# Optimization experiments

Measured on AMD Instinct MI355X. Metric: run time of the kernel, lower is better.

Reference implementation:

```python
import jax, jax.numpy as jnp
import numpy as np

B, T, D, H, K = 128, 64, 2048, 512, 512
WINDOWS = [2, 3, 4]
ROUT = 2 * H            # bidirectional GRU output dim = 1024
FIN = ROUT + len(WINDOWS) * K + 2048 + 1024  # 5632 ('full' concat)
FOUT = 2048
BN_EPS = 1e-5


def setup_inputs() -> dict:
    key = jax.random.key(0)
    ks = jax.random.split(key, 32)
    s = 0.02
    inp = {
        "videos": jax.random.normal(ks[0], (B, T, D), jnp.float32),
        "motions": jax.random.normal(ks[1], (B, 1024), jnp.float32),
        "videos_origin": jax.random.normal(ks[2], (B, 2048), jnp.float32),
        "lengths": jax.random.randint(ks[3], (B,), 1, T + 1, jnp.int32),
        # GRU params (PyTorch layout: gates ordered r,z,n stacked on dim 0)
        "Wih_f": jax.random.normal(ks[4], (3 * H, D), jnp.float32) * s,
        "Whh_f": jax.random.normal(ks[5], (3 * H, H), jnp.float32) * s,
        "bih_f": jnp.zeros((3 * H,), jnp.float32),
        "bhh_f": jnp.zeros((3 * H,), jnp.float32),
        "Wih_b": jax.random.normal(ks[6], (3 * H, D), jnp.float32) * s,
        "Whh_b": jax.random.normal(ks[7], (3 * H, H), jnp.float32) * s,
        "bih_b": jnp.zeros((3 * H,), jnp.float32),
        "bhh_b": jnp.zeros((3 * H,), jnp.float32),
        # FC + BatchNorm1d (eval-mode) of MFC
        "fc_w": jax.random.normal(ks[8], (FOUT, FIN), jnp.float32) * (np.sqrt(6.0) / np.sqrt(FIN + FOUT)),
        "fc_b": jnp.zeros((FOUT,), jnp.float32),
        "bn_gamma": jnp.ones((FOUT,), jnp.float32),
        "bn_beta": jnp.zeros((FOUT,), jnp.float32),
        "bn_mean": jnp.zeros((FOUT,), jnp.float32),
        "bn_var": jnp.ones((FOUT,), jnp.float32),
    }
    for i, ws in enumerate(WINDOWS):
        inp[f"conv_w{ws}"] = jax.random.normal(ks[10 + 2 * i], (K, 1, ws, ROUT), jnp.float32) * s
        inp[f"conv_b{ws}"] = jnp.zeros((K,), jnp.float32)
    # mask consistent with lengths: mask[b,t] = t < lengths[b]
    inp["videos_mask"] = (jnp.arange(T)[None, :] < inp["lengths"][:, None]).astype(jnp.float32)
    return inp


def _gru_dir(x, Wih, Whh, bih, bhh, reverse):
    # x: [B,T,D] -> outputs [B,T,H]; torch GRU cell with r,z,n gate order
    xg = jnp.einsum("btd,gd->btg", x, Wih) + bih  # [B,T,3H] precomputed input gates

    def step(h, xg_t):
        hg = h @ Whh.T + bhh
        xr, xz, xn = jnp.split(xg_t, 3, axis=-1)
        hr, hz, hn = jnp.split(hg, 3, axis=-1)
        r = jax.nn.sigmoid(xr + hr)
        z = jax.nn.sigmoid(xz + hz)
        n = jnp.tanh(xn + r * hn)
        h_new = (1.0 - z) * n + z * h
        return h_new, h_new

    h0 = jnp.zeros((x.shape[0], Whh.shape[1]), x.dtype)
    _, hs = jax.lax.scan(step, h0, jnp.swapaxes(xg, 0, 1), reverse=reverse)
    return jnp.swapaxes(hs, 0, 1)


def _conv_branch(x4, w, b, ws):
    # x4: [B,1,T,ROUT], w: [K,1,ws,ROUT]; torch padding=(ws-1, 0)
    y = jax.lax.conv_general_dilated(
        x4, w, (1, 1), [(ws - 1, ws - 1), (0, 0)],
        dimension_numbers=("NCHW", "OIHW", "NCHW"))  # [B,K,T+ws-1,1]
    y = jax.nn.relu(y + b[None, :, None, None])
    return jnp.max(y, axis=(2, 3))  # max_pool1d over full time -> [B,K]


def _forward(videos, motions, videos_origin, lengths, videos_mask,
             Wih_f, Whh_f, bih_f, bhh_f, Wih_b, Whh_b, bih_b, bhh_b,
             conv_w2, conv_b2, conv_w3, conv_b3, conv_w4, conv_b4,
             fc_w, fc_b, bn_gamma, bn_beta, bn_mean, bn_var):
    fwd = _gru_dir(videos, Wih_f, Whh_f, bih_f, bhh_f, reverse=False)
    bwd = _gru_dir(videos, Wih_b, Whh_b, bih_b, bhh_b, reverse=True)
    gru_init_out = jnp.concatenate([fwd, bwd], axis=-1)  # [B,T,2H]

    # masked mean over valid frames (vectorized version of the batch for-loop)
    denom = lengths.astype(gru_init_out.dtype)[:, None]
    gru_out = jnp.sum(gru_init_out * videos_mask[:, :, None], axis=1) / denom  # [B,2H]

    masked = gru_init_out * videos_mask[:, :, None]
    x4 = masked[:, None, :, :]  # [B,1,T,2H]
    con_out = jnp.concatenate([
        _conv_branch(x4, conv_w2, conv_b2, 2),
        _conv_branch(x4, conv_w3, conv_b3, 3),
        _conv_branch(x4, conv_w4, conv_b4, 4),
    ], axis=1)  # [B,3K]

    # concate == 'full' (dropout is identity in eval)
    features = jnp.concatenate([gru_out, con_out, videos_origin, motions], axis=1)
    features = features @ fc_w.T + fc_b
    # BatchNorm1d, eval mode with running stats
    features = bn_gamma * (features - bn_mean) * jax.lax.rsqrt(bn_var + BN_EPS) + bn_beta
    # l2norm over dim 1
    features = features / jnp.sqrt(jnp.sum(features * features, axis=1, keepdims=True))
    return features


def reference(videos, motions, videos_origin, lengths, videos_mask,
              Wih_f, Whh_f, bih_f, bhh_f, Wih_b, Whh_b, bih_b, bhh_b,
              conv_w2, conv_b2, conv_w3, conv_b3, conv_w4, conv_b4,
              fc_w, fc_b, bn_gamma, bn_beta, bn_mean, bn_var):
    return _forward(videos, motions, videos_origin, lengths, videos_mask,
                    Wih_f, Whh_f, bih_f, bhh_f, Wih_b, Whh_b, bih_b, bhh_b,
                    conv_w2, conv_b2, conv_w3, conv_b3, conv_w4, conv_b4,
                    fc_w, fc_b, bn_gamma, bn_beta, bn_mean, bn_var)
```

## Files before the change

kernel.cpp:

```cpp
#include <hip/hip_runtime.h>
#include <hip/hip_bf16.h>
#include <stdint.h>

typedef __attribute__((ext_vector_type(8))) short short8;
typedef __attribute__((ext_vector_type(4))) float floatx4;
typedef __attribute__((ext_vector_type(4))) unsigned int u32x4;
typedef unsigned short u16;
typedef unsigned int u32;
typedef unsigned long long u64;

static __device__ __forceinline__ u16 f2bf(float f) {
  union { float f; u32 u; } v; v.f = f;
  return (u16)((v.u + 0x7fffu + ((v.u >> 16) & 1u)) >> 16);
}
static __device__ __forceinline__ float bf2f(u16 h) {
  union { u32 u; float f; } v; v.u = ((u32)h) << 16; return v.f;
}
static __device__ __forceinline__ u64 pack4(float a, float b, float c, float d) {
  return (u64)f2bf(a) | ((u64)f2bf(b) << 16) | ((u64)f2bf(c) << 32) | ((u64)f2bf(d) << 48);
}

__global__ __launch_bounds__(256) void k_pre_cvt(
    const float* __restrict__ videos, const float* __restrict__ Wih_f,
    const float* __restrict__ Wih_b, const float* __restrict__ Whh_f,
    const float* __restrict__ Whh_b, const float* __restrict__ bih_f,
    const float* __restrict__ bih_b, const float* __restrict__ fcb,
    const float* __restrict__ gam, const float* __restrict__ bet,
    const float* __restrict__ mu, const float* __restrict__ var,
    u16* __restrict__ vid, u16* __restrict__ wih, u16* __restrict__ whh,
    float* __restrict__ bihcat, float* __restrict__ bns, float* __restrict__ bnt)
{
  const int O1 = 4194304;
  const int O2 = O1 + 786432;
  const int O3 = O2 + 786432;
  const int O4 = O3 + 196608;
  const int O5 = O4 + 196608;
  const int NQ = O5 + 1280;
  for (int q = blockIdx.x * 256 + threadIdx.x; q < NQ; q += gridDim.x * 256) {
    if (q < O1) {
      float4 v = ((const float4*)videos)[q];
      ((u64*)vid)[q] = pack4(v.x, v.y, v.z, v.w);
    } else if (q < O2) {
      int r = q - O1; float4 v = ((const float4*)Wih_f)[r];
      ((u64*)wih)[r] = pack4(v.x, v.y, v.z, v.w);
    } else if (q < O3) {
      int r = q - O2; float4 v = ((const float4*)Wih_b)[r];
      ((u64*)wih)[r + 786432] = pack4(v.x, v.y, v.z, v.w);
    } else if (q < O4) {
      int r = q - O3; float4 v = ((const float4*)Whh_f)[r];
      ((u64*)whh)[r] = pack4(v.x, v.y, v.z, v.w);
    } else if (q < O5) {
      int r = q - O4; float4 v = ((const float4*)Whh_b)[r];
      ((u64*)whh)[r + 196608] = pack4(v.x, v.y, v.z, v.w);
    } else {
      int r = q - O5;
      if (r < 768) {
        int i = r * 4;
        const float* s = (i < 1536) ? (bih_f + i) : (bih_b + (i - 1536));
        *(float4*)&bihcat[i] = *(const float4*)s;
      } else {
        int i = (r - 768) * 4;
#pragma unroll
        for (int j = 0; j < 4; ++j) {
          int idx = i + j;
          float sc = gam[idx] * rsqrtf(var[idx] + 1e-5f);
          bns[idx] = sc;
          bnt[idx] = sc * (fcb[idx] - mu[idx]) + bet[idx];
        }
      }
    }
  }
}

static __device__ __forceinline__ void gload_lds16(const u16* g, u16* l) {
  __builtin_amdgcn_global_load_lds((const __attribute__((address_space(1))) u32*)(const void*)g,
                                   (__attribute__((address_space(3))) u32*)(void*)l, 16, 0, 0);
}

static __device__ __forceinline__ void stage_half_256(
    const u16* __restrict__ Mat, long K, int rowbase, int ktile, u16* lregion,
    int tid, int wid)
{
  int srow = tid >> 3;
  int sce = (((tid >> 3) ^ tid) & 7) * 8;
  const u16* g0 = Mat + (long)(rowbase + srow) * K + ktile * 64 + sce;
  const u16* g1 = Mat + (long)(rowbase + 64 + srow) * K + ktile * 64 + sce;
  gload_lds16(g0, lregion + wid * 512);
  gload_lds16(g1, lregion + 4096 + wid * 512);
}

__global__ __launch_bounds__(512) void gemm256(
    const u16* __restrict__ A, const u16* __restrict__ Bm,
    float* __restrict__ C, u16* __restrict__ C16, int M, int N, int K, int NT,
    const float* __restrict__ shift)
{
  __shared__ u16 lds[65536];
  int tid = threadIdx.x, lane = tid & 63, wid = tid >> 6;
  int r16 = lane & 15, kq = lane >> 4;
  int wr = wid >> 2, wc = wid & 3;
  int nwg = gridDim.x * gridDim.y;
  int lin = blockIdx.y * gridDim.x + blockIdx.x;
  int q8 = nwg >> 3;
  int swz = (lin & 7) * q8 + (lin >> 3);
  int m0 = (swz / gridDim.x) * 256, n0 = (swz % gridDim.x) * 256;

  int fxor = (r16 & 7) << 4;
  int c0 = (kq * 16) ^ fxor;
  int c1 = c0 ^ 64;
  int brow0 = (wc & 1) * 64;
  const char* ldsc = (const char*)lds;

  const floatx4 z4 = {0.f, 0.f, 0.f, 0.f};
  floatx4 acc[8][4];
#pragma unroll
  for (int i = 0; i < 8; ++i)
#pragma unroll
    for (int j = 0; j < 4; ++j) acc[i][j] = z4;

  stage_half_256(Bm, K, n0,       0, lds,                 tid, wid);
  stage_half_256(Bm, K, n0 + 128, 0, lds + 8192,          tid, wid);
  stage_half_256(A,  K, m0,       0, lds + 16384,         tid, wid);
  stage_half_256(A,  K, m0 + 128, 0, lds + 24576,         tid, wid);
  stage_half_256(Bm, K, n0,       1, lds + 32768,         tid, wid);
  stage_half_256(Bm, K, n0 + 128, 1, lds + 32768 + 8192,  tid, wid);
  stage_half_256(A,  K, m0,       1, lds + 32768 + 16384, tid, wid);
  stage_half_256(A,  K, m0 + 128, 1, lds + 32768 + 24576, tid, wid);
  asm volatile("s_waitcnt vmcnt(8)" ::: "memory");
  asm volatile("s_barrier" ::: "memory");

#define MFMA_CLUSTER(q)                                                        \
  asm volatile("s_waitcnt lgkmcnt(0)" ::: "memory");                           \
  __builtin_amdgcn_sched_barrier(0);                                           \
  __builtin_amdgcn_s_setprio(1);                                               \
  _Pragma("unroll")                                                            \
  for (int s = 0; s < 2; ++s)                                                  \
    _Pragma("unroll")                                                          \
    for (int e = 0; e < 2; ++e)                                                \
      _Pragma("unroll")                                                        \
      for (int j = 0; j < 4; ++j)                                              \
        acc[(q)*2 + e][j] = __builtin_amdgcn_mfma_f32_16x16x32_bf16(           \
            af[e][s], bf[j][s], acc[(q)*2 + e][j], 0, 0, 0);                   \
  __builtin_amdgcn_s_setprio(0);

  for (int T = 0; T < NT; ++T) {
    int P = T & 1;
    int Tn1 = (T + 1 < NT) ? T + 1 : 0;
    int Tn2 = (T + 2 < NT) ? T + 2 : T + 2 - NT;
    const char* bbase = ldsc + P * 65536 + (wc >> 1) * 16384;
    const char* abase = ldsc + P * 65536 + 32768 + wr * 16384;
    short8 bf[4][2];
    {
#pragma unroll
      for (int j = 0; j < 4; ++j) {
        bf[j][0] = *(const short8*)(bbase + (brow0 + j * 16 + r16) * 128 + c0);
        bf[j][1] = *(const short8*)(bbase + (brow0 + j * 16 + r16) * 128 + c1);
      }
      short8 af[2][2];
#pragma unroll
      for (int e = 0; e < 2; ++e) {
        af[e][0] = *(const short8*)(abase + (e * 16 + r16) * 128 + c0);
        af[e][1] = *(const short8*)(abase + (e * 16 + r16) * 128 + c1);
      }
      stage_half_256(A, K, m0, Tn1, lds + (Tn1 & 1) * 32768 + 16384, tid, wid);
      asm volatile("s_barrier" ::: "memory");
      MFMA_CLUSTER(0)
      asm volatile("s_barrier" ::: "memory");
    }
    {
      short8 af[2][2];
#pragma unroll
      for (int e = 0; e < 2; ++e) {
        af[e][0] = *(const short8*)(abase + ((2 + e) * 16 + r16) * 128 + c0);
        af[e][1] = *(const short8*)(abase + ((2 + e) * 16 + r16) * 128 + c1);
      }
      stage_half_256(A, K, m0 + 128, Tn1, lds + (Tn1 & 1) * 32768 + 24576, tid, wid);
      asm volatile("s_barrier" ::: "memory");
      MFMA_CLUSTER(1)
      asm volatile("s_barrier" ::: "memory");
    }
    {
      short8 af[2][2];
#pragma unroll
      for (int e = 0; e < 2; ++e) {
        af[e][0] = *(const short8*)(abase + ((4 + e) * 16 + r16) * 128 + c0);
        af[e][1] = *(const short8*)(abase + ((4 + e) * 16 + r16) * 128 + c1);
      }
      stage_half_256(Bm, K, n0, Tn2, lds + P * 32768, tid, wid);
      asm volatile("s_barrier" ::: "memory");
      MFMA_CLUSTER(2)
      asm volatile("s_barrier" ::: "memory");
    }
    {
      short8 af[2][2];
#pragma unroll
      for (int e = 0; e < 2; ++e) {
        af[e][0] = *(const short8*)(abase + ((6 + e) * 16 + r16) * 128 + c0);
        af[e][1] = *(const short8*)(abase + ((6 + e) * 16 + r16) * 128 + c1);
      }
      stage_half_256(Bm, K, n0 + 128, Tn2, lds + P * 32768 + 8192, tid, wid);
      asm volatile("s_barrier" ::: "memory");
      MFMA_CLUSTER(3)
      asm volatile("s_waitcnt vmcnt(4)" ::: "memory");
      asm volatile("s_barrier" ::: "memory");
    }
  }
#undef MFMA_CLUSTER

#pragma unroll
  for (int mf = 0; mf < 8; ++mf)
#pragma unroll
    for (int j = 0; j < 4; ++j) {
      int col = n0 + wc * 64 + j * 16 + r16;
      int row = m0 + wr * 128 + mf * 16 + kq * 4;
      if (C16) {
#pragma unroll
        for (int qq = 0; qq < 4; ++qq)
          C16[(long)(row + qq) * N + col] = f2bf(acc[mf][j][qq]);
      } else {
        float sh = shift ? shift[col] : 0.f;
#pragma unroll
        for (int qq = 0; qq < 4; ++qq)
          C[(long)(row + qq) * N + col] = acc[mf][j][qq] + sh;
      }
    }
}

__global__ __launch_bounds__(256) void gemm_bt(
    const u16* __restrict__ A, const u16* __restrict__ Bm,
    float* __restrict__ C, u16* __restrict__ C16, int M, int N, int K, int kn,
    const float* __restrict__ scale, const float* __restrict__ shift)
{
  __shared__ u16 As[128 * 32];
  __shared__ u16 Bs[128 * 32];
  int tid = threadIdx.x, lane = tid & 63, wid = tid >> 6;
  int nwg = gridDim.x * gridDim.y;
  int lin = blockIdx.y * gridDim.x + blockIdx.x;
  int q8 = nwg >> 3;
  int swz = (lin & 7) * q8 + (lin >> 3);
  int m0 = (swz / gridDim.x) * 128, n0 = (swz % gridDim.x) * 128;
  int kt0 = blockIdx.z * kn;
  int wr = wid >> 1, wc = wid & 1;
  int r16 = lane & 15, kq = lane >> 4;
  const floatx4 z4 = {0.f, 0.f, 0.f, 0.f};
  floatx4 acc[4][4];
#pragma unroll
  for (int i = 0; i < 4; ++i)
#pragma unroll
    for (int j = 0; j < 4; ++j) acc[i][j] = z4;
  for (int kt = kt0; kt < kt0 + kn; ++kt) {
    __syncthreads();
#pragma unroll
    for (int inst = 0; inst < 2; ++inst) {
      int g = inst * 256 + tid;
      int row = g >> 2, cb = g & 3;
      const u16* ga = A + (long)(m0 + row) * K + kt * 32 + cb * 8;
      const u16* gb = Bm + (long)(n0 + row) * K + kt * 32 + cb * 8;
      gload_lds16(ga, &As[(inst * 256 + wid * 64) * 8]);
      gload_lds16(gb, &Bs[(inst * 256 + wid * 64) * 8]);
    }
    __syncthreads();
    short8 af[4], bf[4];
#pragma unroll
    for (int mt = 0; mt < 4; ++mt) af[mt] = *(const short8*)&As[(wr * 64 + mt * 16 + r16) * 32 + kq * 8];
#pragma unroll
    for (int nt = 0; nt < 4; ++nt) bf[nt] = *(const short8*)&Bs[(wc * 64 + nt * 16 + r16) * 32 + kq * 8];
#pragma unroll
    for (int mt = 0; mt < 4; ++mt)
#pragma unroll
      for (int nt = 0; nt < 4; ++nt)
        acc[mt][nt] = __builtin_amdgcn_mfma_f32_16x16x32_bf16(af[mt], bf[nt], acc[mt][nt], 0, 0, 0);
  }
  float* Cp = C + (long)blockIdx.z * M * N;
#pragma unroll
  for (int nt = 0; nt < 4; ++nt) {
    int col = n0 + wc * 64 + nt * 16 + r16;
    float sc = scale ? scale[col] : 1.f;
    float sh = shift ? shift[col] : 0.f;
#pragma unroll
    for (int mt = 0; mt < 4; ++mt)
#pragma unroll
      for (int q = 0; q < 4; ++q) {
        int row = m0 + wr * 64 + mt * 16 + kq * 4 + q;
        float v = acc[mt][nt][q] * sc + sh;
        if (C16) C16[(long)row * N + col] = f2bf(v);
        else     Cp[(long)row * N + col] = v;
      }
  }
}

__global__ __launch_bounds__(512) void gru_rec(
    const float* __restrict__ xg,
    const u16* __restrict__ whhb,
    const float* __restrict__ bhh_f, const float* __restrict__ bhh_b,
    u16* __restrict__ hbuf,
    u16* __restrict__ maskb,
    u16* __restrict__ feat,
    const int* __restrict__ lengths,
    int* __restrict__ flg,
    const float* __restrict__ fc_w, const float* __restrict__ w2,
    const float* __restrict__ w3, const float* __restrict__ w4,
    const float* __restrict__ vo, const float* __restrict__ mo,
    u16* __restrict__ fcw, u16* __restrict__ wc)
{
  __shared__ float part[2][4][3][256];
  __shared__ u16 hstage[8192];
  int tid = threadIdx.x, lane = tid & 63, wid = tid >> 6;
  int bid = blockIdx.x;

  if (bid >= 128) {
    int cid = bid - 128;
    const int C1 = 2883584;
    const int C2 = C1 + 1179648;
    const int C3 = C2 + 65536;
    const int NQ = C3 + 32768;
    for (int q = cid * 512 + tid; q < NQ; q += 128 * 512) {
      if (q < C1) {
        float4 v = ((const float4*)fc_w)[q];
        ((u64*)fcw)[q] = pack4(v.x, v.y, v.z, v.w);
      } else if (q < C2) {
        int r = q - C1;
        int e = r << 2;
        int row = e >> 10, col = e & 1023;
        const float* src;
        if (row < 1024)      { int j = row >> 9, k = row & 511;                 src = w2 + (k * 2 + j) * 1024; }
        else if (row < 2560) { int m = row - 1024; int j = m >> 9, k = m & 511; src = w3 + (k * 3 + j) * 1024; }
        else                 { int m = row - 2560; int j = m >> 9, k = m & 511; src = w4 + (k * 4 + j) * 1024; }
        float4 v = *(const float4*)(src + col);
        ((u64*)wc)[r] = pack4(v.x, v.y, v.z, v.w);
      } else if (q < C3) {
        int r = q - C2; int b = r >> 9, c = (r & 511) * 4;
        float4 v = *(const float4*)&vo[(long)b * 2048 + c];
        *(u64*)&feat[(long)b * 5632 + 2560 + c] = pack4(v.x, v.y, v.z, v.w);
      } else {
        int r = q - C3; int b = r >> 8, c = (r & 255) * 4;
        float4 v = *(const float4*)&mo[(long)b * 1024 + c];
        *(u64*)&feat[(long)b * 5632 + 4608 + c] = pack4(v.x, v.y, v.z, v.w);
      }
    }
    return;
  }

  int dir = bid >> 6, rem = bid & 63, bt = rem >> 3, is = rem & 7;
  int ih = wid & 3, ks = wid >> 2;
  int gbase = (dir * 8 + bt) * 32;
  int r16 = lane & 15, kq = lane >> 4;
  int iglob = is * 64 + ih * 16 + r16;
  int i0 = is * 64 + ih * 16 + kq * 4;
  int batch = bt * 16 + r16;
  int pollidx = gbase + (lane & 31);
  int pubidx = gbase + is * 4 + ih;
  const float* bhh = dir ? bhh_b : bhh_f;
  const floatx4 z4 = {0.f, 0.f, 0.f, 0.f};
  int len = lengths[batch];

  short8 wfrag[3][8];
#pragma unroll
  for (int g = 0; g < 3; ++g) {
    const u16* wrow = whhb + (long)(dir * 1536 + g * 512 + iglob) * 512;
#pragma unroll
    for (int kk = 0; kk < 8; ++kk)
      wfrag[g][kk] = *(const short8*)&wrow[(ks * 8 + kk) * 32 + kq * 8];
  }
  float4 bh4[3];
#pragma unroll
  for (int g = 0; g < 3; ++g) bh4[g] = *(const float4*)&bhh[g * 512 + i0];
  float4 hprev = {0.f, 0.f, 0.f, 0.f};
  float4 msum = {0.f, 0.f, 0.f, 0.f};

  float4 px[3];
  if (ks == 0) {
    int ts0 = dir ? 63 : 0;
    long xb = (long)(batch * 64 + ts0) * 3072 + dir * 1536 + i0;
#pragma unroll
    for (int g = 0; g < 3; ++g) px[g] = *(const float4*)&xg[xb + g * 512];
  }

  int so0 = wid * 2048 + lane * 16;
  int so1 = so0 + 1024;
  char* sl0 = (char*)hstage + (so0 ^ (((so0 >> 10) & 7) << 4));
  char* sl1 = (char*)hstage + (so1 ^ (((so1 >> 10) & 7) << 4));
  int rb = r16 * 1024 + ks * 512 + kq * 16;
  int rsw = (r16 & 7) << 4;

  for (int t = 0; t < 64; ++t) {
    if (t > 0) {
      if (wid == 0) {
        while (true) {
          int v;
          asm volatile("global_load_dword %0, %1, off sc0 sc1\n\ts_waitcnt vmcnt(0)"
                       : "=v"(v) : "v"(&flg[pollidx]) : "memory");
          if (__all(v >= t)) break;
          __builtin_amdgcn_s_sleep(1);
        }
      }
      asm volatile("s_barrier" ::: "memory");
    }
    int par = t & 1;
    const char* hsrc = (const char*)(hbuf + (long)((par * 2 + dir) * 128 + bt * 16) * 512);
    u32x4 qa, qb;
    asm volatile(
      "global_load_dwordx4 %0, %2, off sc0 sc1\n\t"
      "global_load_dwordx4 %1, %3, off sc0 sc1"
      : "=&v"(qa), "=&v"(qb)
      : "v"(hsrc + so0), "v"(hsrc + so1)
      : "memory");
    asm volatile("s_waitcnt vmcnt(0)" ::: "memory");
    *(u32x4*)sl0 = qa;
    *(u32x4*)sl1 = qb;
    float4 pxn[3];
    if (ks == 0 && t < 63) {
      int ts1 = dir ? (62 - t) : (t + 1);
      long xb = (long)(batch * 64 + ts1) * 3072 + dir * 1536 + i0;
#pragma unroll
      for (int g = 0; g < 3; ++g) pxn[g] = *(const float4*)&xg[xb + g * 512];
    }
    asm volatile("s_waitcnt lgkmcnt(0)\n\ts_barrier" ::: "memory");
    floatx4 acc[3];
#pragma unroll
    for (int g = 0; g < 3; ++g) acc[g] = z4;
#pragma unroll
    for (int kk = 0; kk < 8; ++kk) {
      short8 hv = *(const short8*)((const char*)hstage + ((rb + kk * 64) ^ rsw));
#pragma unroll
      for (int g = 0; g < 3; ++g)
        acc[g] = __builtin_amdgcn_mfma_f32_16x16x32_bf16(wfrag[g][kk], hv, acc[g], 0, 0, 0);
    }
    if (ks == 1) {
#pragma unroll
      for (int g = 0; g < 3; ++g) *(floatx4*)&part[par][ih][g][lane * 4] = acc[g];
    }
    asm volatile("s_waitcnt lgkmcnt(0)\n\ts_barrier" ::: "memory");
    if (ks == 0) {
      int tsrc = dir ? (63 - t) : t;
#pragma unroll
      for (int g = 0; g < 3; ++g) acc[g] += *(const floatx4*)&part[par][ih][g][lane * 4];
      float4 hn4;
#pragma unroll
      for (int q = 0; q < 4; ++q) {
        float rr = acc[0][q] + ((const float*)&bh4[0])[q] + ((const float*)&px[0])[q];
        float zz = acc[1][q] + ((const float*)&bh4[1])[q] + ((const float*)&px[1])[q];
        float r = 1.f / (1.f + __expf(-rr));
        float z = 1.f / (1.f + __expf(-zz));
        float n = tanhf(((const float*)&px[2])[q] + r * (acc[2][q] + ((const float*)&bh4[2])[q]));
        ((float*)&hn4)[q] = (1.f - z) * n + z * ((const float*)&hprev)[q];
      }
      hprev = hn4;
      u16* hdst = hbuf + (long)(((par ^ 1) * 2 + dir) * 128 + bt * 16) * 512;
      u64 hval = pack4(hn4.x, hn4.y, hn4.z, hn4.w);
      asm volatile("global_atomic_swap_x2 %0, %1, off sc1"
                   :: "v"((u64*)&hdst[r16 * 512 + i0]), "v"(hval) : "memory");
      if (t < 63) {
        asm volatile("s_waitcnt vmcnt(0)" ::: "memory");
        if (lane == 0) {
          int tv = t + 1;
          asm volatile("global_atomic_swap %0, %1, off sc1"
                       :: "v"(&flg[pubidx]), "v"(tv) : "memory");
        }
      }
      bool mv = tsrc < len;
      *(u64*)&maskb[(long)(batch * 64 + tsrc) * 1024 + dir * 512 + i0] = mv ? hval : 0ull;
      if (mv) {
        msum.x += hn4.x; msum.y += hn4.y; msum.z += hn4.z; msum.w += hn4.w;
      }
      px[0] = pxn[0]; px[1] = pxn[1]; px[2] = pxn[2];
    }
  }
  if (ks == 0) {
    float inv = 1.0f / (float)len;
    *(u64*)&feat[(long)batch * 5632 + dir * 512 + i0] =
        pack4(msum.x * inv, msum.y * inv, msum.z * inv, msum.w * inv);
  }
}

__global__ __launch_bounds__(256) void k_conv_finish(
    const u16* __restrict__ z, const float* __restrict__ cb2,
    const float* __restrict__ cb3, const float* __restrict__ cb4,
    u16* __restrict__ feat)
{
  int b = blockIdx.x, wsi = blockIdx.y, k2 = threadIdx.x * 2;
  int ws = wsi + 2;
  int base = (wsi == 0) ? 0 : (wsi == 1 ? 1024 : 2560);
  const float* cb = (wsi == 0) ? cb2 : (wsi == 1 ? cb3 : cb4);
  float bias0 = cb[k2], bias1 = cb[k2 + 1];
  float m0 = 0.f, m1 = 0.f;
  for (int p = 0; p < 64 + ws - 1; ++p) {
    float a0 = bias0, a1 = bias1;
    for (int j = 0; j < ws; ++j) {
      int t = p - (ws - 1) + j;
      if (t >= 0 && t < 64) {
        u32 v = *(const u32*)&z[(long)(b * 64 + t) * 4608 + base + j * 512 + k2];
        a0 += bf2f((u16)v);
        a1 += bf2f((u16)(v >> 16));
      }
    }
    m0 = fmaxf(m0, a0);
    m1 = fmaxf(m1, a1);
  }
  *(u32*)&feat[(long)b * 5632 + 1024 + wsi * 512 + k2] = (u32)f2bf(m0) | ((u32)f2bf(m1) << 16);
}

__global__ __launch_bounds__(256) void k_l2norm(const float* __restrict__ p,
    const float* __restrict__ bns, const float* __restrict__ bnt, float* __restrict__ out)
{
  __shared__ float red[4];
  int b = blockIdx.x, tid = threadIdx.x;
  float v[8]; float s = 0.f;
#pragma unroll
  for (int j = 0; j < 8; ++j) {
    int i = j * 256 + tid;
    long o = (long)b * 2048 + i;
    float a = 0.f;
#pragma unroll
    for (int zz = 0; zz < 8; ++zz) a += p[o + (long)zz * 262144];
    a = a * bns[i] + bnt[i];
    v[j] = a; s += a * a;
  }
#pragma unroll
  for (int o = 32; o > 0; o >>= 1) s += __shfl_down(s, o);
  if ((tid & 63) == 0) red[tid >> 6] = s;
  __syncthreads();
  float rn = rsqrtf(red[0] + red[1] + red[2] + red[3]);
#pragma unroll
  for (int j = 0; j < 8; ++j)
    out[(long)b * 2048 + j * 256 + tid] = v[j] * rn;
}

extern "C" void kernel_launch(void* const* d_in, const int* in_sizes, int n_in,
                              void* d_out, int out_size, void* d_ws, size_t ws_size,
                              hipStream_t stream)
{
  (void)in_sizes; (void)n_in; (void)out_size; (void)ws_size;
  const float* videos       = (const float*)d_in[0];
  const float* motions      = (const float*)d_in[1];
  const float* videos_origin= (const float*)d_in[2];
  const int*   lengths      = (const int*)d_in[3];
  const float* Wih_f = (const float*)d_in[4];
  const float* Whh_f = (const float*)d_in[5];
  const float* bih_f = (const float*)d_in[6];
  const float* bhh_f = (const float*)d_in[7];
  const float* Wih_b = (const float*)d_in[8];
  const float* Whh_b = (const float*)d_in[9];
  const float* bih_b = (const float*)d_in[10];
  const float* bhh_b = (const float*)d_in[11];
  const float* fc_w  = (const float*)d_in[12];
  const float* fc_b  = (const float*)d_in[13];
  const float* bn_gamma = (const float*)d_in[14];
  const float* bn_beta  = (const float*)d_in[15];
  const float* bn_mean  = (const float*)d_in[16];
  const float* bn_var   = (const float*)d_in[17];
  const float* conv_w2 = (const float*)d_in[18];
  const float* conv_b2 = (const float*)d_in[19];
  const float* conv_w3 = (const float*)d_in[20];
  const float* conv_b3 = (const float*)d_in[21];
  const float* conv_w4 = (const float*)d_in[22];
  const float* conv_b4 = (const float*)d_in[23];
  float* out = (float*)d_out;
  char* w = (char*)d_ws;

  const size_t XG    = 0;
  const size_t VID   = 134217728;
  const size_t MASKB = 167772160;
  const size_t WIH   = 184549376;
  const size_t WHH   = 197132288;
  const size_t WC    = 200278016;
  const size_t FCW   = 209715200;
  const size_t FEAT  = 232783872;
  const size_t BIH   = 235274240;
  const size_t BNS   = 235286528;
  const size_t BNT   = 235294720;
  const size_t HB    = 235302912;
  const size_t FLG   = HB + 524288;

  float* xg   = (float*)(w + XG);
  u16*   zb16 = (u16*)(w + XG);
  u16* vid    = (u16*)(w + VID);
  u16* maskb  = (u16*)(w + MASKB);
  float* fcp  = (float*)(w + MASKB);
  u16* wih    = (u16*)(w + WIH);
  u16* whh    = (u16*)(w + WHH);
  u16* wc_    = (u16*)(w + WC);
  u16* fcw    = (u16*)(w + FCW);
  u16* feat   = (u16*)(w + FEAT);
  float* bih  = (float*)(w + BIH);
  float* bns  = (float*)(w + BNS);
  float* bnt  = (float*)(w + BNT);
  u16* hb     = (u16*)(w + HB);
  int* flg    = (int*)(w + FLG);

  hipMemsetAsync(w + HB, 0, 524288 + 2048, stream);

  k_pre_cvt<<<4096, 256, 0, stream>>>(
      videos, Wih_f, Wih_b, Whh_f, Whh_b, bih_f, bih_b,
      fc_b, bn_gamma, bn_beta, bn_mean, bn_var,
      vid, wih, whh, bih, bns, bnt);

  gemm256<<<dim3(12, 32), 512, 0, stream>>>(vid, wih, xg, nullptr, 8192, 3072, 2048, 32, bih);

  {
    const float* xg_c = xg; const u16* whh_c = whh;
    u16* hb_c = hb; u16* mb_c = maskb; u16* ft_c = feat;
    const int* len_c = lengths; int* flg_c = flg;
    const float* bf_c = bhh_f; const float* bb_c = bhh_b;
    const float* fw_c = fc_w; const float* w2_c = conv_w2;
    const float* w3_c = conv_w3; const float* w4_c = conv_w4;
    const float* vo_c = videos_origin; const float* mo_c = motions;
    u16* fcw_c = fcw; u16* wc_c = wc_;
    void* args[] = { (void*)&xg_c, (void*)&whh_c, (void*)&bf_c, (void*)&bb_c,
                     (void*)&hb_c, (void*)&mb_c, (void*)&ft_c, (void*)&len_c, (void*)&flg_c,
                     (void*)&fw_c, (void*)&w2_c, (void*)&w3_c, (void*)&w4_c,
                     (void*)&vo_c, (void*)&mo_c, (void*)&fcw_c, (void*)&wc_c };
    hipLaunchCooperativeKernel(reinterpret_cast<void*>(gru_rec), dim3(256), dim3(512), args, 0, stream);
  }

  gemm256<<<dim3(18, 32), 512, 0, stream>>>(maskb, wc_, nullptr, zb16, 8192, 4608, 1024, 16, nullptr);
  k_conv_finish<<<dim3(128, 3), 256, 0, stream>>>(zb16, conv_b2, conv_b3, conv_b4, feat);
  gemm_bt<<<dim3(16, 1, 8), 256, 0, stream>>>(feat, fcw, fcp, nullptr, 128, 2048, 5632, 22, nullptr, nullptr);
  k_l2norm<<<128, 256, 0, stream>>>(fcp, bns, bnt, out);
}
```

Baseline: 592.7 us.

## Tag hidden-state words with step counter to replace separate flag polling

The GRU recurrence previously published each step's hidden state and then, after a vmcnt wait, a separate per-group flag that consumers polled before loading the state. Now every 32-bit pair of bf16 hidden values is stored alongside its step tag in one 64-bit atomic swap. Consumers spin directly on the data loads until all tags match the current step. This removes the wait-then-flag round trip and the separate poll from the critical path of each serial step, at the cost of doubling the hidden-state buffer size and having all threads spin on data.

```diff
diff --git a/kernel.cpp b/kernel.cpp
--- a/kernel.cpp
+++ b/kernel.cpp
@@ -292,11 +292,10 @@
     const float* __restrict__ xg,
     const u16* __restrict__ whhb,
     const float* __restrict__ bhh_f, const float* __restrict__ bhh_b,
-    u16* __restrict__ hbuf,
+    char* __restrict__ hb3,
     u16* __restrict__ maskb,
     u16* __restrict__ feat,
     const int* __restrict__ lengths,
-    int* __restrict__ flg,
     const float* __restrict__ fc_w, const float* __restrict__ w2,
     const float* __restrict__ w3, const float* __restrict__ w4,
     const float* __restrict__ vo, const float* __restrict__ mo,
@@ -342,13 +341,10 @@
 
   int dir = bid >> 6, rem = bid & 63, bt = rem >> 3, is = rem & 7;
   int ih = wid & 3, ks = wid >> 2;
-  int gbase = (dir * 8 + bt) * 32;
   int r16 = lane & 15, kq = lane >> 4;
   int iglob = is * 64 + ih * 16 + r16;
   int i0 = is * 64 + ih * 16 + kq * 4;
   int batch = bt * 16 + r16;
-  int pollidx = gbase + (lane & 31);
-  int pubidx = gbase + is * 4 + ih;
   const float* bhh = dir ? bhh_b : bhh_f;
   const floatx4 z4 = {0.f, 0.f, 0.f, 0.f};
   int len = lengths[batch];
@@ -375,38 +371,46 @@
     for (int g = 0; g < 3; ++g) px[g] = *(const float4*)&xg[xb + g * 512];
   }
 
-  int so0 = wid * 2048 + lane * 16;
-  int so1 = so0 + 1024;
-  char* sl0 = (char*)hstage + (so0 ^ (((so0 >> 10) & 7) << 4));
-  char* sl1 = (char*)hstage + (so1 ^ (((so1 >> 10) & 7) << 4));
+  char* slot[2];
+  slot[0] = hb3 + (long)((0 * 2 + dir) * 8 + bt) * 32768;
+  slot[1] = hb3 + (long)((1 * 2 + dir) * 8 + bt) * 32768;
+  char* sdst[4];
+#pragma unroll
+  for (int k = 0; k < 4; ++k) {
+    int row = 4 * k + (tid >> 7);
+    int colb = (tid & 127) * 8;
+    sdst[k] = (char*)hstage + row * 1024 + (colb ^ ((row & 7) << 4));
+  }
+  int ld_off = tid * 16;
+  int p0 = r16 * 256 + is * 32 + ih * 8 + kq * 2;
   int rb = r16 * 1024 + ks * 512 + kq * 16;
   int rsw = (r16 & 7) << 4;
 
   for (int t = 0; t < 64; ++t) {
-    if (t > 0) {
-      if (wid == 0) {
-        while (true) {
-          int v;
-          asm volatile("global_load_dword %0, %1, off sc0 sc1\n\ts_waitcnt vmcnt(0)"
-                       : "=v"(v) : "v"(&flg[pollidx]) : "memory");
-          if (__all(v >= t)) break;
-          __builtin_amdgcn_s_sleep(1);
-        }
-      }
-      asm volatile("s_barrier" ::: "memory");
-    }
     int par = t & 1;
-    const char* hsrc = (const char*)(hbuf + (long)((par * 2 + dir) * 128 + bt * 16) * 512);
-    u32x4 qa, qb;
-    asm volatile(
-      "global_load_dwordx4 %0, %2, off sc0 sc1\n\t"
-      "global_load_dwordx4 %1, %3, off sc0 sc1"
-      : "=&v"(qa), "=&v"(qb)
-      : "v"(hsrc + so0), "v"(hsrc + so1)
-      : "memory");
-    asm volatile("s_waitcnt vmcnt(0)" ::: "memory");
-    *(u32x4*)sl0 = qa;
-    *(u32x4*)sl1 = qb;
+    u32 tg = (u32)t;
+    const char* sb = slot[par];
+    u32x4 L0, L1, L2, L3;
+    while (true) {
+      asm volatile(
+        "global_load_dwordx4 %0, %4, off sc0 sc1\n\t"
+        "global_load_dwordx4 %1, %5, off sc0 sc1\n\t"
+        "global_load_dwordx4 %2, %6, off sc0 sc1\n\t"
+        "global_load_dwordx4 %3, %7, off sc0 sc1\n\t"
+        "s_waitcnt vmcnt(0)"
+        : "=&v"(L0), "=&v"(L1), "=&v"(L2), "=&v"(L3)
+        : "v"(sb + ld_off), "v"(sb + 8192 + ld_off),
+          "v"(sb + 16384 + ld_off), "v"(sb + 24576 + ld_off)
+        : "memory");
+      bool ok = (L0.y == tg) & (L0.w == tg) & (L1.y == tg) & (L1.w == tg) &
+                (L2.y == tg) & (L2.w == tg) & (L3.y == tg) & (L3.w == tg);
+      if (ok) break;
+      __builtin_amdgcn_s_sleep(1);
+    }
+    *(u64*)sdst[0] = (u64)L0.x | ((u64)L0.z << 32);
+    *(u64*)sdst[1] = (u64)L1.x | ((u64)L1.z << 32);
+    *(u64*)sdst[2] = (u64)L2.x | ((u64)L2.z << 32);
+    *(u64*)sdst[3] = (u64)L3.x | ((u64)L3.z << 32);
     float4 pxn[3];
     if (ks == 0 && t < 63) {
       int ts1 = dir ? (62 - t) : (t + 1);
@@ -445,17 +449,16 @@
         ((float*)&hn4)[q] = (1.f - z) * n + z * ((const float*)&hprev)[q];
       }
       hprev = hn4;
-      u16* hdst = hbuf + (long)(((par ^ 1) * 2 + dir) * 128 + bt * 16) * 512;
       u64 hval = pack4(hn4.x, hn4.y, hn4.z, hn4.w);
-      asm volatile("global_atomic_swap_x2 %0, %1, off sc1"
-                   :: "v"((u64*)&hdst[r16 * 512 + i0]), "v"(hval) : "memory");
       if (t < 63) {
-        asm volatile("s_waitcnt vmcnt(0)" ::: "memory");
-        if (lane == 0) {
-          int tv = t + 1;
-          asm volatile("global_atomic_swap %0, %1, off sc1"
-                       :: "v"(&flg[pubidx]), "v"(tv) : "memory");
-        }
+        u32 tg1 = (u32)(t + 1);
+        char* pb = slot[(t + 1) & 1] + p0 * 8;
+        u64 v0 = (u64)(u32)hval | ((u64)tg1 << 32);
+        u64 v1 = (u64)(u32)(hval >> 32) | ((u64)tg1 << 32);
+        asm volatile("global_atomic_swap_x2 %0, %1, off sc1"
+                     :: "v"(pb), "v"(v0) : "memory");
+        asm volatile("global_atomic_swap_x2 %0, %1, off sc1"
+                     :: "v"(pb + 8), "v"(v1) : "memory");
       }
       bool mv = tsrc < len;
       *(u64*)&maskb[(long)(batch * 64 + tsrc) * 1024 + dir * 512 + i0] = mv ? hval : 0ull;
@@ -558,6 +561,7 @@
   char* w = (char*)d_ws;
 
   const size_t XG    = 0;
+  const size_t HS    = 100663296;
   const size_t VID   = 134217728;
   const size_t MASKB = 167772160;
   const size_t WIH   = 184549376;
@@ -568,11 +572,10 @@
   const size_t BIH   = 235274240;
   const size_t BNS   = 235286528;
   const size_t BNT   = 235294720;
-  const size_t HB    = 235302912;
-  const size_t FLG   = HB + 524288;
 
   float* xg   = (float*)(w + XG);
   u16*   zb16 = (u16*)(w + XG);
+  char* hb3   = (char*)(w + HS);
   u16* vid    = (u16*)(w + VID);
   u16* maskb  = (u16*)(w + MASKB);
   float* fcp  = (float*)(w + MASKB);
@@ -584,10 +587,8 @@
   float* bih  = (float*)(w + BIH);
   float* bns  = (float*)(w + BNS);
   float* bnt  = (float*)(w + BNT);
-  u16* hb     = (u16*)(w + HB);
-  int* flg    = (int*)(w + FLG);
-
-  hipMemsetAsync(w + HB, 0, 524288 + 2048, stream);
+
+  hipMemsetAsync(hb3, 0, 1048576, stream);
 
   k_pre_cvt<<<4096, 256, 0, stream>>>(
       videos, Wih_f, Wih_b, Whh_f, Whh_b, bih_f, bih_b,
@@ -598,15 +599,15 @@
 
   {
     const float* xg_c = xg; const u16* whh_c = whh;
-    u16* hb_c = hb; u16* mb_c = maskb; u16* ft_c = feat;
-    const int* len_c = lengths; int* flg_c = flg;
+    char* hb_c = hb3; u16* mb_c = maskb; u16* ft_c = feat;
+    const int* len_c = lengths;
     const float* bf_c = bhh_f; const float* bb_c = bhh_b;
     const float* fw_c = fc_w; const float* w2_c = conv_w2;
     const float* w3_c = conv_w3; const float* w4_c = conv_w4;
     const float* vo_c = videos_origin; const float* mo_c = motions;
     u16* fcw_c = fcw; u16* wc_c = wc_;
     void* args[] = { (void*)&xg_c, (void*)&whh_c, (void*)&bf_c, (void*)&bb_c,
-                     (void*)&hb_c, (void*)&mb_c, (void*)&ft_c, (void*)&len_c, (void*)&flg_c,
+                     (void*)&hb_c, (void*)&mb_c, (void*)&ft_c, (void*)&len_c,
                      (void*)&fw_c, (void*)&w2_c, (void*)&w3_c, (void*)&w4_c,
                      (void*)&vo_c, (void*)&mo_c, (void*)&fcw_c, (void*)&wc_c };
     hipLaunchCooperativeKernel(reinterpret_cast<void*>(gru_rec), dim3(256), dim3(512), args, 0, stream);
```

Result: faster. 560.5 us (-5.4%).
